# Kernel tuning notes

Hardware: AMD Instinct MI355X
Metric: run time of the kernel (lower is better)

The kernel has to match this reference:

```python
import jax, jax.numpy as jnp
import numpy as np

B, N, DIM = 4, 1024, 1024
HEADS, DH = 16, 64
INNER = HEADS * DH          # 1024
PROJ_H = max(16, DH // 8)   # 16
TOP_K = 256
TEMP = 1.0
SCALE = DH ** -0.5
LN_EPS = 1e-5


def setup_inputs() -> dict:
    key = jax.random.key(0)
    ks = jax.random.split(key, 9)
    s = 0.02
    return {
        "x": jax.random.normal(ks[0], (B, N, DIM), dtype=jnp.float32),
        "w_qkv": jax.random.normal(ks[1], (3 * INNER, DIM), dtype=jnp.float32) * s,
        "w_out": jax.random.normal(ks[2], (DIM, INNER), dtype=jnp.float32) * s,
        "b_out": jnp.zeros((DIM,), dtype=jnp.float32),
        "ln_g": jnp.ones((DH,), dtype=jnp.float32),
        "ln_b": jnp.zeros((DH,), dtype=jnp.float32),
        "w1": jax.random.normal(ks[3], (PROJ_H, DH), dtype=jnp.float32) * s,
        "b1": jnp.zeros((PROJ_H,), dtype=jnp.float32),
        "w2": jax.random.normal(ks[4], (1, PROJ_H), dtype=jnp.float32) * s,
        "b2": jnp.zeros((1,), dtype=jnp.float32),
    }


def _soma_gate(token_feat, ln_g, ln_b, w1, b1, w2, b2):
    # token_feat: [B, N, DH] -> gate [B, N] in (0,1)
    mu = token_feat.mean(axis=-1, keepdims=True)
    var = token_feat.var(axis=-1, keepdims=True)
    H = (token_feat - mu) * jax.lax.rsqrt(var + LN_EPS) * ln_g + ln_b
    h = jax.nn.gelu(H @ w1.T + b1, approximate=False)
    scores = (h @ w2.T + b2)[..., 0]                       # [B, N]
    scores = scores / (TEMP + 1e-12)
    # top-k soft mask: non-topk positions set to -1e9 before sigmoid
    topk_vals, topk_idx = jax.lax.top_k(scores, TOP_K)
    b_idx = jnp.arange(scores.shape[0])[:, None]
    scores = jnp.full_like(scores, -1e9).at[b_idx, topk_idx].set(topk_vals)
    return jax.nn.sigmoid(scores)


def reference(x, w_qkv, w_out, b_out, ln_g, ln_b, w1, b1, w2, b2):
    Bx, Nx, _ = x.shape
    qkv = x @ w_qkv.T                                      # [B, N, 3*INNER]
    q, k, v = jnp.split(qkv, 3, axis=-1)
    to_heads = lambda t: t.reshape(Bx, Nx, HEADS, DH).transpose(0, 2, 1, 3)
    q, k, v = to_heads(q), to_heads(k), to_heads(v)        # [B, H, N, DH]

    dots = jnp.einsum('bhid,bhjd->bhij', q, k) * SCALE     # [B, H, N, N]

    q_mean = q.mean(axis=1)                                # [B, N, DH]
    gate = _soma_gate(q_mean, ln_g, ln_b, w1, b1, w2, b2)  # [B, N]
    dots = dots * (gate[:, None, :, None] * gate[:, None, None, :])

    attn = jax.nn.softmax(dots, axis=-1)
    out = jnp.einsum('bhij,bhjd->bhid', attn, v)           # [B, H, N, DH]
    out = out.transpose(0, 2, 1, 3).reshape(Bx, Nx, INNER)
    return out @ w_out.T + b_out
```

## Files before the change

### kernel.cpp

```cpp
#include <hip/hip_runtime.h>
#include <hip/hip_bf16.h>
#include <stdint.h>

typedef __bf16 bf16;
typedef __bf16 bf16x8 __attribute__((ext_vector_type(8)));
typedef float floatx4 __attribute__((ext_vector_type(4)));

typedef const __attribute__((address_space(1))) uint32_t glb_u32;
typedef __attribute__((address_space(3))) uint32_t lds_u32;

__device__ __forceinline__ void cp16(void* lds, const void* gp) {
    __builtin_amdgcn_global_load_lds((glb_u32*)gp, (lds_u32*)lds, 16, 0, 0);
}

#define MFMA16(a, b, c) __builtin_amdgcn_mfma_f32_16x16x32_bf16((a), (b), (c), 0, 0, 0)
#define SCALE_ 0.125f

__global__ __launch_bounds__(256) void k_cvt_prep(
    const float* __restrict__ x, const float* __restrict__ wq,
    const float* __restrict__ wo, bf16* __restrict__ xb,
    bf16* __restrict__ xl, bf16* __restrict__ wqb, bf16* __restrict__ wob,
    bf16* __restrict__ whl, float* __restrict__ xsum) {
    __shared__ float red[4][64];
    if (blockIdx.x < 4096) {
        size_t i8 = ((size_t)blockIdx.x * 256 + threadIdx.x) * 8;
        const float* src; bf16* dst; size_t off; bool isx = false;
        if (i8 < 4194304)      { src = x;  dst = xb;  off = i8; isx = true; }
        else if (i8 < 7340032) { src = wq; dst = wqb; off = i8 - 4194304; }
        else                   { src = wo; dst = wob; off = i8 - 7340032; }
        float4 a = *(const float4*)(src + off);
        float4 b = *(const float4*)(src + off + 4);
        union { bf16 h[8]; uint4 u; } hi, lo;
        hi.h[0] = (bf16)a.x; hi.h[1] = (bf16)a.y; hi.h[2] = (bf16)a.z; hi.h[3] = (bf16)a.w;
        hi.h[4] = (bf16)b.x; hi.h[5] = (bf16)b.y; hi.h[6] = (bf16)b.z; hi.h[7] = (bf16)b.w;
        *(uint4*)(dst + off) = hi.u;
        if (isx) {
            lo.h[0] = (bf16)(a.x - (float)hi.h[0]);
            lo.h[1] = (bf16)(a.y - (float)hi.h[1]);
            lo.h[2] = (bf16)(a.z - (float)hi.h[2]);
            lo.h[3] = (bf16)(a.w - (float)hi.h[3]);
            lo.h[4] = (bf16)(b.x - (float)hi.h[4]);
            lo.h[5] = (bf16)(b.y - (float)hi.h[5]);
            lo.h[6] = (bf16)(b.z - (float)hi.h[6]);
            lo.h[7] = (bf16)(b.w - (float)hi.h[7]);
            *(uint4*)(xl + off) = lo.u;
        }
    } else if (blockIdx.x < 4352) {
        int t = (blockIdx.x - 4096) * 256 + threadIdx.x;
        int k = t & 1023, d = t >> 10;
        float s = 0.f;
        #pragma unroll
        for (int h = 0; h < 16; ++h) s += wq[(size_t)(h * 64 + d) * 1024 + k];
        s *= (1.f / 16.f);
        bf16 hi = (bf16)s;
        whl[(size_t)d * 1024 + k] = hi;
        whl[(size_t)(64 + d) * 1024 + k] = (bf16)(s - (float)hi);
    } else {
        int j = blockIdx.x - 4352;
        int b = j >> 4, c0 = (j & 15) << 6;
        int lane = threadIdx.x & 63, q = threadIdx.x >> 6;
        const float* p = x + (size_t)b * 1048576 + (size_t)q * 262144 + c0 + lane;
        float s = 0.f;
        #pragma unroll 8
        for (int n = 0; n < 256; ++n) s += p[(size_t)n * 1024];
        red[q][lane] = s;
        __syncthreads();
        if (threadIdx.x < 64)
            xsum[b * 1024 + c0 + threadIdx.x] =
                red[0][threadIdx.x] + red[1][threadIdx.x] +
                red[2][threadIdx.x] + red[3][threadIdx.x];
    }
}

__global__ __launch_bounds__(256) void k_score_gemm(
    const bf16* __restrict__ xh, const bf16* __restrict__ xl,
    const bf16* __restrict__ whl, const float* __restrict__ lng,
    const float* __restrict__ lnb, const float* __restrict__ w1f,
    const float* __restrict__ b1f, const float* __restrict__ w2f,
    const float* __restrict__ b2f, float* __restrict__ scores) {
    __shared__ bf16 Ah[128 * 32];
    __shared__ bf16 Al[128 * 32];
    __shared__ bf16 Bs[128 * 32];
    __shared__ float Sbuf[128][65];
    __shared__ float Hs[4][64];
    const int t = threadIdx.x;
    const int lane = t & 63;
    const int w = t >> 6;
    const int m0 = blockIdx.x * 128;
    const int srow = t >> 2;
    const int scol = (t & 3) * 8;
    const int fr = lane & 15;
    const int kc = (lane >> 4) * 8;
    const int wm0 = w * 32;

    floatx4 zero4 = {0.f, 0.f, 0.f, 0.f};
    floatx4 acc[2][4];
    #pragma unroll
    for (int i = 0; i < 2; ++i)
        #pragma unroll
        for (int j = 0; j < 4; ++j) acc[i][j] = zero4;

    for (int k0 = 0; k0 < 1024; k0 += 32) {
        __syncthreads();
        cp16(Ah + t * 8,        xh + (size_t)(m0 + srow) * 1024 + k0 + scol);
        cp16(Ah + t * 8 + 2048, xh + (size_t)(m0 + srow + 64) * 1024 + k0 + scol);
        cp16(Al + t * 8,        xl + (size_t)(m0 + srow) * 1024 + k0 + scol);
        cp16(Al + t * 8 + 2048, xl + (size_t)(m0 + srow + 64) * 1024 + k0 + scol);
        cp16(Bs + t * 8,        whl + (size_t)srow * 1024 + k0 + scol);
        cp16(Bs + t * 8 + 2048, whl + (size_t)(srow + 64) * 1024 + k0 + scol);
        __syncthreads();
        bf16x8 ah[2], al[2], bh[4], bl[4];
        #pragma unroll
        for (int mi = 0; mi < 2; ++mi) {
            ah[mi] = *(const bf16x8*)&Ah[(wm0 + mi * 16 + fr) * 32 + kc];
            al[mi] = *(const bf16x8*)&Al[(wm0 + mi * 16 + fr) * 32 + kc];
        }
        #pragma unroll
        for (int ni = 0; ni < 4; ++ni) {
            bh[ni] = *(const bf16x8*)&Bs[(ni * 16 + fr) * 32 + kc];
            bl[ni] = *(const bf16x8*)&Bs[(64 + ni * 16 + fr) * 32 + kc];
        }
        #pragma unroll
        for (int mi = 0; mi < 2; ++mi)
            #pragma unroll
            for (int ni = 0; ni < 4; ++ni) {
                acc[mi][ni] = MFMA16(ah[mi], bh[ni], acc[mi][ni]);
                acc[mi][ni] = MFMA16(ah[mi], bl[ni], acc[mi][ni]);
                acc[mi][ni] = MFMA16(al[mi], bh[ni], acc[mi][ni]);
            }
    }

    const int rowb = (lane >> 4) * 4;
    #pragma unroll
    for (int mi = 0; mi < 2; ++mi)
        #pragma unroll
        for (int ni = 0; ni < 4; ++ni)
            #pragma unroll
            for (int r = 0; r < 4; ++r)
                Sbuf[wm0 + mi * 16 + rowb + r][ni * 16 + fr] = acc[mi][ni][r];

    const int p = lane & 15, q = lane >> 4;
    float w1r[16];
    #pragma unroll
    for (int j = 0; j < 16; ++j) w1r[j] = w1f[p * 64 + q * 16 + j];
    const float b1r = b1f[p], w2r = w2f[p], b2r = b2f[0];
    const float lgr = lng[lane], lbr = lnb[lane];
    __syncthreads();
    for (int rr = 0; rr < 32; ++rr) {
        const int row = w * 32 + rr;
        float qm = Sbuf[row][lane];
        float s = qm;
        #pragma unroll
        for (int off = 32; off > 0; off >>= 1) s += __shfl_xor(s, off);
        float mu = s * (1.f / 64.f);
        float dx = qm - mu;
        float v2 = dx * dx;
        #pragma unroll
        for (int off = 32; off > 0; off >>= 1) v2 += __shfl_xor(v2, off);
        float var = v2 * (1.f / 64.f);
        float H = dx * (1.0f / sqrtf(var + 1e-5f)) * lgr + lbr;
        Hs[w][lane] = H;
        float pa = 0.f;
        #pragma unroll
        for (int j = 0; j < 16; ++j) pa += Hs[w][q * 16 + j] * w1r[j];
        pa += __shfl_xor(pa, 16);
        pa += __shfl_xor(pa, 32);
        float a = pa + b1r;
        float g = 0.5f * a * (1.0f + erff(a * 0.70710678118654752f));
        float sc = g * w2r;
        #pragma unroll
        for (int off = 1; off < 16; off <<= 1) sc += __shfl_xor(sc, off);
        if (lane == 0) scores[m0 + row] = sc + b2r;
    }
}

__global__ __launch_bounds__(256) void k_topk(const float* __restrict__ scores,
                                              float* __restrict__ gate,
                                              int* __restrict__ idx,
                                              float* __restrict__ gsel) {
    const int w = threadIdx.x >> 6, lane = threadIdx.x & 63;
    const float* sc = scores + w * 1024;
    float s[16];
    uint32_t key[16];
    #pragma unroll
    for (int i = 0; i < 16; ++i) {
        s[i] = sc[lane * 16 + i];
        uint32_t u = __float_as_uint(s[i]);
        key[i] = (u >> 31) ? ~u : (u | 0x80000000u);
    }
    uint32_t prefix = 0;
    for (int bit = 31; bit >= 0; --bit) {
        uint32_t cand = prefix | (1u << bit);
        int c = 0;
        #pragma unroll
        for (int i = 0; i < 16; ++i) c += (key[i] >= cand);
        #pragma unroll
        for (int off = 1; off < 64; off <<= 1) c += __shfl_xor(c, off);
        if (c >= 256) prefix = cand;
    }
    int cg = 0, eq = 0;
    #pragma unroll
    for (int i = 0; i < 16; ++i) { cg += (key[i] > prefix); eq += (key[i] == prefix); }
    #pragma unroll
    for (int off = 1; off < 64; off <<= 1) cg += __shfl_xor(cg, off);
    const int quota = 256 - cg;
    int xs = eq;
    #pragma unroll
    for (int off = 1; off < 64; off <<= 1) {
        int y = __shfl_up(xs, off);
        if (lane >= off) xs += y;
    }
    int run = xs - eq;
    bool selv[16];
    int cnt = 0;
    #pragma unroll
    for (int i = 0; i < 16; ++i) {
        bool sel = key[i] > prefix;
        if (key[i] == prefix) { sel = (run < quota); run++; }
        selv[i] = sel;
        cnt += sel ? 1 : 0;
        gate[w * 1024 + lane * 16 + i] = sel ? 1.0f / (1.0f + expf(-s[i])) : 0.0f;
    }
    int xc = cnt;
    #pragma unroll
    for (int off = 1; off < 64; off <<= 1) {
        int y = __shfl_up(xc, off);
        if (lane >= off) xc += y;
    }
    int pos = xc - cnt;
    #pragma unroll
    for (int i = 0; i < 16; ++i) {
        if (selv[i]) {
            idx[w * 256 + pos]  = lane * 16 + i;
            gsel[w * 256 + pos] = 1.0f / (1.0f + expf(-s[i]));
            pos++;
        }
    }
}

__global__ __launch_bounds__(256) void k_qkv_sel(
    const bf16* __restrict__ xb, const bf16* __restrict__ wqb,
    const int* __restrict__ idx, bf16* __restrict__ qsel,
    bf16* __restrict__ ksel, bf16* __restrict__ VselT,
    const float* __restrict__ xsum, float* __restrict__ meanVbuf) {
    __shared__ bf16 As[128 * 32];
    __shared__ bf16 Bs[128 * 32];
    __shared__ float xsS[1024];
    const int t = threadIdx.x;

    if (blockIdx.x >= 192) {
        const int j = blockIdx.x - 192, b = j >> 2, kq = j & 3;
        for (int k = t; k < 1024; k += 256) xsS[k] = xsum[b * 1024 + k];
        __syncthreads();
        const int k2 = kq * 256 + t;
        const bf16* wr = wqb + (size_t)(2048 + k2) * 1024;
        float s = 0.f;
        for (int k = 0; k < 1024; k += 8) {
            bf16x8 v = *(const bf16x8*)(wr + k);
            #pragma unroll
            for (int jj = 0; jj < 8; ++jj) s += (float)v[jj] * xsS[k + jj];
        }
        meanVbuf[b * 1024 + k2] = s * (1.f / 1024.f);
        return;
    }

    const int lane = t & 63;
    const int w = t >> 6;
    const int srow = t >> 2;
    const int scol = (t & 3) * 8;
    const int wm = (w & 1) * 64;
    const int wn = (w >> 1) * 64;
    const int fr = lane & 15;
    const int kc = (lane >> 4) * 8;

    const int bid = blockIdx.x;
    const int n0 = (bid % 24) * 128;
    const int m0 = (bid / 24) * 128;
    const bf16* Bsrc = wqb + (size_t)n0 * 1024;
    const int mg1 = m0 + srow, mg2 = mg1 + 64;
    const int tok1 = idx[(mg1 >> 8) * 256 + (mg1 & 255)];
    const int tok2 = idx[(mg2 >> 8) * 256 + (mg2 & 255)];
    const size_t abase1 = ((size_t)(mg1 >> 8) * 1024 + tok1) * 1024;
    const size_t abase2 = ((size_t)(mg2 >> 8) * 1024 + tok2) * 1024;

    floatx4 zero4 = {0.f, 0.f, 0.f, 0.f};
    floatx4 acc[4][4];
    #pragma unroll
    for (int i = 0; i < 4; ++i)
        #pragma unroll
        for (int j = 0; j < 4; ++j) acc[i][j] = zero4;

    for (int k0 = 0; k0 < 1024; k0 += 32) {
        __syncthreads();
        cp16(As + t * 8,        xb + abase1 + k0 + scol);
        cp16(As + t * 8 + 2048, xb + abase2 + k0 + scol);
        cp16(Bs + t * 8,        Bsrc + (size_t)srow * 1024 + k0 + scol);
        cp16(Bs + t * 8 + 2048, Bsrc + (size_t)(srow + 64) * 1024 + k0 + scol);
        __syncthreads();
        bf16x8 a[4], b[4];
        #pragma unroll
        for (int mi = 0; mi < 4; ++mi)
            a[mi] = *(const bf16x8*)&As[(wm + mi * 16 + fr) * 32 + kc];
        #pragma unroll
        for (int ni = 0; ni < 4; ++ni)
            b[ni] = *(const bf16x8*)&Bs[(wn + ni * 16 + fr) * 32 + kc];
        #pragma unroll
        for (int mi = 0; mi < 4; ++mi)
            #pragma unroll
            for (int ni = 0; ni < 4; ++ni)
                acc[mi][ni] = MFMA16(a[mi], b[ni], acc[mi][ni]);
    }

    const int rowb = (lane >> 4) * 4;
    #pragma unroll
    for (int ni = 0; ni < 4; ++ni) {
        const int n_base = n0 + wn + ni * 16;
        const int region = n_base >> 10;
        const int nn = n_base & 1023;
        const int h = nn >> 6;
        const int dd = (nn & 63) + fr;
        if (region < 2) {
            #pragma unroll
            for (int mi = 0; mi < 4; ++mi)
                #pragma unroll
                for (int r = 0; r < 4; ++r) {
                    const int mg = m0 + wm + mi * 16 + rowb + r;
                    const bf16 v = (bf16)acc[mi][ni][r];
                    if (region == 0) {
                        qsel[(size_t)mg * 1024 + h * 64 + dd] = v;
                    } else {
                        const int b = mg >> 8, s = mg & 255;
                        ksel[(((size_t)(b * 16 + h)) * 256 + s) * 64 + dd] = v;
                    }
                }
        } else {
            #pragma unroll
            for (int mi = 0; mi < 4; ++mi) {
                const int mgb = m0 + wm + mi * 16 + rowb;
                const int b = mgb >> 8, s0 = mgb & 255;
                union { bf16 h4[4]; uint2 u; } pk;
                #pragma unroll
                for (int r = 0; r < 4; ++r) pk.h4[r] = (bf16)acc[mi][ni][r];
                *(uint2*)&VselT[(((size_t)(b * 16 + h)) * 64 + dd) * 256 + s0] = pk.u;
            }
        }
    }
}

__global__ __launch_bounds__(256) void k_attn(
    bf16* __restrict__ qsel, const bf16* __restrict__ Ksel,
    const bf16* __restrict__ VselT, const float* __restrict__ gsel,
    const float* __restrict__ meanVbuf, const bf16* __restrict__ wob,
    const float* __restrict__ b_out, float* __restrict__ ubase) {
    __shared__ bf16 Qs[64 * 72];
    __shared__ bf16 Ks[64 * 72];
    __shared__ bf16 Vs[64 * 72];
    __shared__ bf16 Ps[4][16 * 72];
    __shared__ float redS[4][64];
    __shared__ float SumV[64];
    __shared__ float mvS[1024];
    const int t = threadIdx.x;

    if (blockIdx.x >= 256) {
        const int j = blockIdx.x - 256, bb = j >> 2, nq = j & 3;
        for (int k = t; k < 1024; k += 256) mvS[k] = meanVbuf[bb * 1024 + k];
        __syncthreads();
        const int n = nq * 256 + t;
        const bf16* wr = wob + (size_t)n * 1024;
        float s = b_out[n];
        for (int k = 0; k < 1024; k += 8) {
            bf16x8 v = *(const bf16x8*)(wr + k);
            #pragma unroll
            for (int jj = 0; jj < 8; ++jj) s += (float)v[jj] * mvS[k + jj];
        }
        ubase[bb * 1024 + n] = s;
        return;
    }

    const int bh = blockIdx.x >> 2;
    const int qt = blockIdx.x & 3;
    const int b = bh >> 4, h = bh & 15;
    const int w = t >> 6, lane = t & 63;
    const int m0 = qt * 64;
    const bf16* kb = Ksel + (size_t)bh * 16384;
    const bf16* vb = VselT + (size_t)bh * 16384;

    #pragma unroll
    for (int c = 0; c < 2; ++c) {
        int idx2 = t + 256 * c, row = idx2 >> 3, c8 = (idx2 & 7) * 8;
        *(uint4*)&Qs[row * 72 + c8] =
            *(const uint4*)&qsel[(size_t)(b * 256 + m0 + row) * 1024 + h * 64 + c8];
    }
    {
        const int dd_ = t & 63, pp_ = t >> 6;
        const bf16* vr = vb + (size_t)dd_ * 256 + pp_ * 64;
        float ss = 0.f;
        #pragma unroll
        for (int k = 0; k < 64; k += 8) {
            bf16x8 v = *(const bf16x8*)(vr + k);
            #pragma unroll
            for (int jj = 0; jj < 8; ++jj) ss += (float)v[jj];
        }
        redS[pp_][dd_] = ss;
    }
    const int fr = lane & 15;
    const int kq = lane >> 4;
    const int rowb = kq * 4;
    __syncthreads();
    if (t < 64)
        SumV[t] = meanVbuf[b * 1024 + h * 64 + t] * 1024.f -
                  (redS[0][t] + redS[1][t] + redS[2][t] + redS[3][t]);
    bf16x8 aq[2];
    aq[0] = *(const bf16x8*)&Qs[(w * 16 + fr) * 72 + kq * 8];
    aq[1] = *(const bf16x8*)&Qs[(w * 16 + fr) * 72 + 32 + kq * 8];

    float gq[4];
    #pragma unroll
    for (int r = 0; r < 4; ++r)
        gq[r] = gsel[b * 256 + m0 + w * 16 + rowb + r] * SCALE_;

    float mrow[4] = {0.f, 0.f, 0.f, 0.f};
    float lrow[4] = {0.f, 0.f, 0.f, 0.f};
    floatx4 zero4 = {0.f, 0.f, 0.f, 0.f};
    floatx4 Of[4] = {zero4, zero4, zero4, zero4};

    for (int jt = 0; jt < 4; ++jt) {
        const int j0 = jt * 64;
        __syncthreads();
        #pragma unroll
        for (int c = 0; c < 2; ++c) {
            int idx2 = t + 256 * c, row = idx2 >> 3, c8 = (idx2 & 7) * 8;
            *(uint4*)&Ks[row * 72 + c8] = *(const uint4*)&kb[(size_t)(j0 + row) * 64 + c8];
            *(uint4*)&Vs[row * 72 + c8] = *(const uint4*)&vb[(size_t)row * 256 + j0 + c8];
        }
        __syncthreads();

        floatx4 S[4] = {zero4, zero4, zero4, zero4};
        #pragma unroll
        for (int ks = 0; ks < 2; ++ks) {
            #pragma unroll
            for (int ni = 0; ni < 4; ++ni) {
                bf16x8 bfr = *(const bf16x8*)&Ks[(ni * 16 + fr) * 72 + ks * 32 + kq * 8];
                S[ni] = MFMA16(aq[ks], bfr, S[ni]);
            }
        }
        float gk[4];
        #pragma unroll
        for (int ni = 0; ni < 4; ++ni) gk[ni] = gsel[b * 256 + j0 + ni * 16 + fr];

        float p[4][4], rmax[4] = {0.f, 0.f, 0.f, 0.f};
        #pragma unroll
        for (int ni = 0; ni < 4; ++ni)
            #pragma unroll
            for (int r = 0; r < 4; ++r) {
                float sv = S[ni][r] * (gq[r] * gk[ni]);
                p[ni][r] = sv;
                rmax[r] = fmaxf(rmax[r], sv);
            }
        #pragma unroll
        for (int r = 0; r < 4; ++r) {
            #pragma unroll
            for (int off = 1; off < 16; off <<= 1)
                rmax[r] = fmaxf(rmax[r], __shfl_xor(rmax[r], off));
        }
        float alpha[4], rsum[4] = {0.f, 0.f, 0.f, 0.f};
        #pragma unroll
        for (int r = 0; r < 4; ++r) {
            float mn = fmaxf(mrow[r], rmax[r]);
            alpha[r] = __expf(mrow[r] - mn);
            mrow[r] = mn;
        }
        #pragma unroll
        for (int ni = 0; ni < 4; ++ni)
            #pragma unroll
            for (int r = 0; r < 4; ++r) {
                float pv = __expf(p[ni][r] - mrow[r]);
                p[ni][r] = pv;
                rsum[r] += pv;
            }
        #pragma unroll
        for (int r = 0; r < 4; ++r) {
            #pragma unroll
            for (int off = 1; off < 16; off <<= 1) rsum[r] += __shfl_xor(rsum[r], off);
            lrow[r] = lrow[r] * alpha[r] + rsum[r];
        }
        #pragma unroll
        for (int nd = 0; nd < 4; ++nd)
            #pragma unroll
            for (int r = 0; r < 4; ++r) Of[nd][r] *= alpha[r];

        #pragma unroll
        for (int ni = 0; ni < 4; ++ni)
            #pragma unroll
            for (int r = 0; r < 4; ++r)
                Ps[w][(rowb + r) * 72 + ni * 16 + fr] = (bf16)p[ni][r];

        #pragma unroll
        for (int ks = 0; ks < 2; ++ks) {
            bf16x8 ap = *(const bf16x8*)&Ps[w][fr * 72 + ks * 32 + kq * 8];
            #pragma unroll
            for (int nd = 0; nd < 4; ++nd) {
                bf16x8 bv = *(const bf16x8*)&Vs[(nd * 16 + fr) * 72 + ks * 32 + kq * 8];
                Of[nd] = MFMA16(ap, bv, Of[nd]);
            }
        }
    }

    #pragma unroll
    for (int nd = 0; nd < 4; ++nd)
        #pragma unroll
        for (int r = 0; r < 4; ++r) {
            float em = __expf(-mrow[r]);
            float num = Of[nd][r] + em * SumV[nd * 16 + fr];
            float den = lrow[r] + 768.0f * em;
            qsel[(size_t)(b * 256 + m0 + w * 16 + rowb + r) * 1024 +
                 h * 64 + nd * 16 + fr] = (bf16)(num / den);
        }
}

__global__ __launch_bounds__(256) void k_out_sel(
    const bf16* __restrict__ A, const bf16* __restrict__ wob,
    const float* __restrict__ b_out, const int* __restrict__ idx,
    const float* __restrict__ ubase, const float* __restrict__ gate,
    float* __restrict__ out) {
    __shared__ bf16 As[128 * 32];
    __shared__ bf16 Bs[128 * 32];
    const int t = threadIdx.x;
    const int gb = blockIdx.x;

    if (gb >= 64) {
        const int fb = gb - 64;
        const int c = t * 4;
        #pragma unroll
        for (int r = 0; r < 4; ++r) {
            const int tokg = fb * 4 + r;
            if (gate[tokg] > 0.f) continue;
            const int b = tokg >> 10;
            *(float4*)(out + (size_t)tokg * 1024 + c) =
                *(const float4*)(ubase + b * 1024 + c);
        }
        return;
    }

    const int lane = t & 63;
    const int w = t >> 6;
    const int n0 = (gb & 7) * 128;
    const int m0 = (gb >> 3) * 128;
    const bf16* Bsrc = wob + (size_t)n0 * 1024;

    const int srow = t >> 2;
    const int scol = (t & 3) * 8;
    const int wm = (w & 1) * 64;
    const int wn = (w >> 1) * 64;
    const int fr = lane & 15;
    const int kc = (lane >> 4) * 8;

    floatx4 zero4 = {0.f, 0.f, 0.f, 0.f};
    floatx4 acc[4][4];
    #pragma unroll
    for (int i = 0; i < 4; ++i)
        #pragma unroll
        for (int j = 0; j < 4; ++j) acc[i][j] = zero4;

    for (int k0 = 0; k0 < 1024; k0 += 32) {
        __syncthreads();
        cp16(As + t * 8,        A + (size_t)(m0 + srow) * 1024 + k0 + scol);
        cp16(As + t * 8 + 2048, A + (size_t)(m0 + srow + 64) * 1024 + k0 + scol);
        cp16(Bs + t * 8,        Bsrc + (size_t)srow * 1024 + k0 + scol);
        cp16(Bs + t * 8 + 2048, Bsrc + (size_t)(srow + 64) * 1024 + k0 + scol);
        __syncthreads();
        bf16x8 a[4], b[4];
        #pragma unroll
        for (int mi = 0; mi < 4; ++mi)
            a[mi] = *(const bf16x8*)&As[(wm + mi * 16 + fr) * 32 + kc];
        #pragma unroll
        for (int ni = 0; ni < 4; ++ni)
            b[ni] = *(const bf16x8*)&Bs[(wn + ni * 16 + fr) * 32 + kc];
        #pragma unroll
        for (int mi = 0; mi < 4; ++mi)
            #pragma unroll
            for (int ni = 0; ni < 4; ++ni)
                acc[mi][ni] = MFMA16(a[mi], b[ni], acc[mi][ni]);
    }

    const int rowb = (lane >> 4) * 4;
    #pragma unroll
    for (int ni = 0; ni < 4; ++ni) {
        const int ng = n0 + wn + ni * 16 + fr;
        const float bias = b_out[ng];
        #pragma unroll
        for (int mi = 0; mi < 4; ++mi)
            #pragma unroll
            for (int r = 0; r < 4; ++r) {
                const int mg = m0 + wm + mi * 16 + rowb + r;
                const float val = acc[mi][ni][r] + bias;
                const int bb = mg >> 8, ss = mg & 255;
                const int tok = idx[bb * 256 + ss];
                out[((size_t)bb * 1024 + tok) * 1024 + ng] = val;
            }
    }
}

extern "C" void kernel_launch(void* const* d_in, const int* in_sizes, int n_in,
                              void* d_out, int out_size, void* d_ws, size_t ws_size,
                              hipStream_t stream) {
    const float* x     = (const float*)d_in[0];
    const float* w_qkv = (const float*)d_in[1];
    const float* w_out = (const float*)d_in[2];
    const float* b_out = (const float*)d_in[3];
    const float* ln_g  = (const float*)d_in[4];
    const float* ln_b  = (const float*)d_in[5];
    const float* w1    = (const float*)d_in[6];
    const float* b1    = (const float*)d_in[7];
    const float* w2    = (const float*)d_in[8];
    const float* b2    = (const float*)d_in[9];
    float* out = (float*)d_out;

    char* ws = (char*)d_ws;
    bf16*  qsel  = (bf16*)(ws);
    bf16*  ksel  = (bf16*)(ws + 4194304);
    bf16*  VselT = (bf16*)(ws + 6291456);
    float* xsum  = (float*)(ws + 8388608);
    bf16*  xb    = (bf16*)(ws + 16777216);
    bf16*  wqb   = (bf16*)(ws + 25165824);
    bf16*  wob   = (bf16*)(ws + 31457280);
    int*   idx      = (int*)(ws + 33554432);
    float* gsel     = (float*)(ws + 33558528);
    float* scores   = (float*)(ws + 33562624);
    float* gate     = (float*)(ws + 33579008);
    float* meanVbuf = (float*)(ws + 33595392);
    float* ubase    = (float*)(ws + 33611776);
    bf16*  whl      = (bf16*)(ws + 33685504);
    bf16*  xlbuf    = (bf16*)(ws + 35651584);

    k_cvt_prep<<<4416, 256, 0, stream>>>(x, w_qkv, w_out, xb, xlbuf, wqb, wob, whl, xsum);
    k_score_gemm<<<32, 256, 0, stream>>>(xb, xlbuf, whl, ln_g, ln_b, w1, b1, w2, b2, scores);
    k_topk<<<1, 256, 0, stream>>>(scores, gate, idx, gsel);
    k_qkv_sel<<<208, 256, 0, stream>>>(xb, wqb, idx, qsel, ksel, VselT, xsum, meanVbuf);
    k_attn<<<272, 256, 0, stream>>>(qsel, ksel, VselT, gsel, meanVbuf, wob, b_out, ubase);
    k_out_sel<<<1088, 256, 0, stream>>>(qsel, wob, b_out, idx, ubase, gate, out);
}
```

Measured before the change: 240.1 us.

## Split score GEMM along K into 512 blocks with separate reduction tail kernel

The score GEMM previously ran on only 32 blocks, each looping over the full K=1024. It now uses 64-row tiles and an 8-way split of K, giving 512 blocks that write fp32 partial sums to workspace. A new tail kernel sums the partials, then applies the layernorm, MLP and gelu to produce the scores. This fills the GPU far better, at the cost of an extra launch and extra global traffic for the partials (about 8 MB). The partials reuse the workspace region later used by qsel/ksel.

```diff
diff --git a/kernel.cpp b/kernel.cpp
--- a/kernel.cpp
+++ b/kernel.cpp
@@ -74,103 +74,91 @@
 
 __global__ __launch_bounds__(256) void k_score_gemm(
     const bf16* __restrict__ xh, const bf16* __restrict__ xl,
-    const bf16* __restrict__ whl, const float* __restrict__ lng,
-    const float* __restrict__ lnb, const float* __restrict__ w1f,
-    const float* __restrict__ b1f, const float* __restrict__ w2f,
-    const float* __restrict__ b2f, float* __restrict__ scores) {
-    __shared__ bf16 Ah[128 * 32];
-    __shared__ bf16 Al[128 * 32];
+    const bf16* __restrict__ whl, float* __restrict__ qm8) {
+    __shared__ bf16 Ah[64 * 32];
+    __shared__ bf16 Al[64 * 32];
     __shared__ bf16 Bs[128 * 32];
-    __shared__ float Sbuf[128][65];
-    __shared__ float Hs[4][64];
     const int t = threadIdx.x;
     const int lane = t & 63;
     const int w = t >> 6;
-    const int m0 = blockIdx.x * 128;
+    const int m0 = (blockIdx.x >> 3) * 64;
+    const int kbase = (blockIdx.x & 7) * 128;
     const int srow = t >> 2;
     const int scol = (t & 3) * 8;
     const int fr = lane & 15;
     const int kc = (lane >> 4) * 8;
-    const int wm0 = w * 32;
 
     floatx4 zero4 = {0.f, 0.f, 0.f, 0.f};
-    floatx4 acc[2][4];
-    #pragma unroll
-    for (int i = 0; i < 2; ++i)
-        #pragma unroll
-        for (int j = 0; j < 4; ++j) acc[i][j] = zero4;
-
-    for (int k0 = 0; k0 < 1024; k0 += 32) {
+    floatx4 acc[4] = {zero4, zero4, zero4, zero4};
+
+    for (int k0 = kbase; k0 < kbase + 128; k0 += 32) {
         __syncthreads();
         cp16(Ah + t * 8,        xh + (size_t)(m0 + srow) * 1024 + k0 + scol);
-        cp16(Ah + t * 8 + 2048, xh + (size_t)(m0 + srow + 64) * 1024 + k0 + scol);
         cp16(Al + t * 8,        xl + (size_t)(m0 + srow) * 1024 + k0 + scol);
-        cp16(Al + t * 8 + 2048, xl + (size_t)(m0 + srow + 64) * 1024 + k0 + scol);
         cp16(Bs + t * 8,        whl + (size_t)srow * 1024 + k0 + scol);
         cp16(Bs + t * 8 + 2048, whl + (size_t)(srow + 64) * 1024 + k0 + scol);
         __syncthreads();
-        bf16x8 ah[2], al[2], bh[4], bl[4];
-        #pragma unroll
-        for (int mi = 0; mi < 2; ++mi) {
-            ah[mi] = *(const bf16x8*)&Ah[(wm0 + mi * 16 + fr) * 32 + kc];
-            al[mi] = *(const bf16x8*)&Al[(wm0 + mi * 16 + fr) * 32 + kc];
-        }
+        bf16x8 ah, al, bh[4], bl[4];
+        ah = *(const bf16x8*)&Ah[(w * 16 + fr) * 32 + kc];
+        al = *(const bf16x8*)&Al[(w * 16 + fr) * 32 + kc];
         #pragma unroll
         for (int ni = 0; ni < 4; ++ni) {
             bh[ni] = *(const bf16x8*)&Bs[(ni * 16 + fr) * 32 + kc];
             bl[ni] = *(const bf16x8*)&Bs[(64 + ni * 16 + fr) * 32 + kc];
         }
         #pragma unroll
-        for (int mi = 0; mi < 2; ++mi)
-            #pragma unroll
-            for (int ni = 0; ni < 4; ++ni) {
-                acc[mi][ni] = MFMA16(ah[mi], bh[ni], acc[mi][ni]);
-                acc[mi][ni] = MFMA16(ah[mi], bl[ni], acc[mi][ni]);
-                acc[mi][ni] = MFMA16(al[mi], bh[ni], acc[mi][ni]);
-            }
+        for (int ni = 0; ni < 4; ++ni) {
+            acc[ni] = MFMA16(ah, bh[ni], acc[ni]);
+            acc[ni] = MFMA16(ah, bl[ni], acc[ni]);
+            acc[ni] = MFMA16(al, bh[ni], acc[ni]);
+        }
     }
 
     const int rowb = (lane >> 4) * 4;
-    #pragma unroll
-    for (int mi = 0; mi < 2; ++mi)
-        #pragma unroll
-        for (int ni = 0; ni < 4; ++ni)
-            #pragma unroll
-            for (int r = 0; r < 4; ++r)
-                Sbuf[wm0 + mi * 16 + rowb + r][ni * 16 + fr] = acc[mi][ni][r];
-
-    const int p = lane & 15, q = lane >> 4;
-    float w1r[16];
-    #pragma unroll
-    for (int j = 0; j < 16; ++j) w1r[j] = w1f[p * 64 + q * 16 + j];
-    const float b1r = b1f[p], w2r = w2f[p], b2r = b2f[0];
-    const float lgr = lng[lane], lbr = lnb[lane];
-    __syncthreads();
-    for (int rr = 0; rr < 32; ++rr) {
-        const int row = w * 32 + rr;
-        float qm = Sbuf[row][lane];
-        float s = qm;
-        #pragma unroll
-        for (int off = 32; off > 0; off >>= 1) s += __shfl_xor(s, off);
-        float mu = s * (1.f / 64.f);
-        float dx = qm - mu;
-        float v2 = dx * dx;
-        #pragma unroll
-        for (int off = 32; off > 0; off >>= 1) v2 += __shfl_xor(v2, off);
-        float var = v2 * (1.f / 64.f);
-        float H = dx * (1.0f / sqrtf(var + 1e-5f)) * lgr + lbr;
-        Hs[w][lane] = H;
-        float pa = 0.f;
-        #pragma unroll
-        for (int j = 0; j < 16; ++j) pa += Hs[w][q * 16 + j] * w1r[j];
-        pa += __shfl_xor(pa, 16);
-        pa += __shfl_xor(pa, 32);
-        float a = pa + b1r;
-        float g = 0.5f * a * (1.0f + erff(a * 0.70710678118654752f));
-        float sc = g * w2r;
-        #pragma unroll
-        for (int off = 1; off < 16; off <<= 1) sc += __shfl_xor(sc, off);
-        if (lane == 0) scores[m0 + row] = sc + b2r;
+    const size_t kofs = (size_t)(blockIdx.x & 7) * 4096;
+    #pragma unroll
+    for (int ni = 0; ni < 4; ++ni)
+        #pragma unroll
+        for (int r = 0; r < 4; ++r)
+            qm8[(kofs + m0 + w * 16 + rowb + r) * 64 + ni * 16 + fr] = acc[ni][r];
+}
+
+__global__ __launch_bounds__(256) void k_score_tail(
+    const float* __restrict__ qm8, const float* __restrict__ lng,
+    const float* __restrict__ lnb, const float* __restrict__ w1f,
+    const float* __restrict__ b1f, const float* __restrict__ w2f,
+    const float* __restrict__ b2f, float* __restrict__ scores) {
+    const int w = threadIdx.x >> 6, lane = threadIdx.x & 63;
+    const int r = blockIdx.x * 4 + w;
+    __shared__ float Hs[4][64];
+    __shared__ float hh[4][16];
+
+    float qm = 0.f;
+    #pragma unroll
+    for (int ks = 0; ks < 8; ++ks)
+        qm += qm8[((size_t)ks * 4096 + r) * 64 + lane];
+    float s = qm;
+    #pragma unroll
+    for (int off = 32; off > 0; off >>= 1) s += __shfl_xor(s, off);
+    float mu = s * (1.f / 64.f);
+    float dx = qm - mu;
+    float v2 = dx * dx;
+    #pragma unroll
+    for (int off = 32; off > 0; off >>= 1) v2 += __shfl_xor(v2, off);
+    float var = v2 * (1.f / 64.f);
+    float H = dx * (1.0f / sqrtf(var + 1e-5f)) * lng[lane] + lnb[lane];
+    Hs[w][lane] = H;
+    if (lane < 16) {
+        float a = b1f[lane];
+        #pragma unroll
+        for (int d = 0; d < 64; ++d) a += Hs[w][d] * w1f[lane * 64 + d];
+        hh[w][lane] = 0.5f * a * (1.0f + erff(a * 0.70710678118654752f));
+    }
+    if (lane == 0) {
+        float sc = b2f[0];
+        #pragma unroll
+        for (int p = 0; p < 16; ++p) sc += hh[w][p] * w2f[p];
+        scores[r] = sc;
     }
 }
 
@@ -620,6 +608,7 @@
     bf16*  qsel  = (bf16*)(ws);
     bf16*  ksel  = (bf16*)(ws + 4194304);
     bf16*  VselT = (bf16*)(ws + 6291456);
+    float* qm8   = (float*)(ws);
     float* xsum  = (float*)(ws + 8388608);
     bf16*  xb    = (bf16*)(ws + 16777216);
     bf16*  wqb   = (bf16*)(ws + 25165824);
@@ -634,7 +623,8 @@
     bf16*  xlbuf    = (bf16*)(ws + 35651584);
 
     k_cvt_prep<<<4416, 256, 0, stream>>>(x, w_qkv, w_out, xb, xlbuf, wqb, wob, whl, xsum);
-    k_score_gemm<<<32, 256, 0, stream>>>(xb, xlbuf, whl, ln_g, ln_b, w1, b1, w2, b2, scores);
+    k_score_gemm<<<512, 256, 0, stream>>>(xb, xlbuf, whl, qm8);
+    k_score_tail<<<1024, 256, 0, stream>>>(qm8, ln_g, ln_b, w1, b1, w2, b2, scores);
     k_topk<<<1, 256, 0, stream>>>(scores, gate, idx, gsel);
     k_qkv_sel<<<208, 256, 0, stream>>>(xb, wqb, idx, qsel, ksel, VselT, xsum, meanVbuf);
     k_attn<<<272, 256, 0, stream>>>(qsel, ksel, VselT, gsel, meanVbuf, wob, b_out, ubase);
```

Result: faster. 201.7 us (-16.0%).
